# Kernel optimization log

Hardware: AMD Instinct MI355X
Metric: run time of the kernel (lower is better)

## Reference

```python
import jax, jax.numpy as jnp
import numpy as np

N_HEADS = 16


def setup_inputs() -> dict:
    key = jax.random.key(0)
    k1, k2, k3, k4, k5 = jax.random.split(key, 5)
    B, S, D = 2, 2048, 1024
    return {
        "query": jax.random.normal(k1, (B, S, D), dtype=jnp.float32),
        "key": jax.random.normal(k2, (B, S, D), dtype=jnp.float32),
        "value": jax.random.normal(k3, (B, S, D), dtype=jnp.float32),
        "fc_w": jax.random.normal(k4, (D, D), dtype=jnp.float32) * (1.0 / np.sqrt(D)),
        "fc_b": jax.random.normal(k5, (D,), dtype=jnp.float32) * 0.01,
    }


def reference(query, key, value, fc_w, fc_b):
    b, s, d = query.shape
    head_dim = d // N_HEADS
    q = query.reshape(b, s, N_HEADS, head_dim)
    k = key.reshape(b, s, N_HEADS, head_dim)
    v = value.reshape(b, s, N_HEADS, head_dim)
    # energy: [b, n, q, k]
    energy = jnp.einsum('bqnd,bknd->bnqk', q, k)
    scale = 1.0 / jnp.sqrt(jnp.asarray(head_dim, dtype=energy.dtype))
    attn = jax.nn.softmax(energy * scale, axis=3)
    out = jnp.einsum('bnqk,bknd->bqnd', attn, v).reshape(b, s, d)
    # fc: y = x @ W^T + b (torch Linear convention)
    return out @ fc_w.T + fc_b
```

## Files before the change

### kernel.cpp

```cpp
#include <hip/hip_runtime.h>
#include <hip/hip_bf16.h>

#define BATCH 2
#define SEQ 2048
#define DMODEL 1024
#define NHEADS 16
#define HDIM 64
#define KVBLK 64
#define NCHUNK (SEQ / KVBLK)
#define NITER (NCHUNK / 2)

#define QSCALE 0.180336880f
#define DEFER_THR 8.0f

typedef __bf16 bf16x8 __attribute__((ext_vector_type(8)));
typedef __bf16 bf16x4 __attribute__((ext_vector_type(4)));
typedef float f32x4 __attribute__((ext_vector_type(4)));
typedef float f32x16 __attribute__((ext_vector_type(16)));
typedef unsigned int uint2v __attribute__((ext_vector_type(2)));

union B8u { unsigned int u[4]; bf16x8 v; };

__device__ __forceinline__ unsigned int cvt_pk_bf16(float lo, float hi) {
  unsigned int d;
  asm("v_cvt_pk_bf16_f32 %0, %1, %2" : "=v"(d) : "v"(lo), "v"(hi));
  return d;
}

__device__ __forceinline__ void permlane32_swap(unsigned &a, unsigned &b) {
  auto r = __builtin_amdgcn_permlane32_swap(a, b, false, false);
  unsigned tmp[2];
  __builtin_memcpy(tmp, &r, 8);
  a = tmp[0]; b = tmp[1];
}

__global__ __launch_bounds__(256)
void conv_all(const float* __restrict__ K, __bf16* __restrict__ Kbf,
              const float* __restrict__ V, __bf16* __restrict__ Vt,
              const float* __restrict__ W, __bf16* __restrict__ Wbf) {
  const int p = blockIdx.x;
  __shared__ __bf16 T[64][72];

  if (p < 2048) {
    const int t = p * 256 + threadIdx.x;
    const int d8 = t & 7, key = (t >> 3) & (SEQ - 1), g = t >> 14;
    const float* src = K + ((size_t)(g >> 4) * SEQ + key) * DMODEL +
                       (g & 15) * HDIM + d8 * 8;
    f32x4 a = *reinterpret_cast<const f32x4*>(src);
    f32x4 c = *reinterpret_cast<const f32x4*>(src + 4);
    bf16x8 o;
#pragma unroll
    for (int j = 0; j < 4; ++j) { o[j] = (__bf16)a[j]; o[4 + j] = (__bf16)c[j]; }
    *reinterpret_cast<bf16x8*>(Kbf + (size_t)t * 8) = o;
  } else if (p < 3072) {
    const int blk = p - 2048;
    const int g = blk >> 5, c0 = (blk & 31) * 64;
    const int b = g >> 4, h = g & 15;
    {
      const int key = threadIdx.x >> 2, dq = threadIdx.x & 3;
      const float* src = V + ((size_t)(b * SEQ) + c0 + key) * DMODEL +
                         h * HDIM + dq * 16;
#pragma unroll
      for (int i = 0; i < 4; ++i) {
        f32x4 v = *reinterpret_cast<const f32x4*>(src + 4 * i);
        bf16x4 o;
#pragma unroll
        for (int j = 0; j < 4; ++j) o[j] = (__bf16)v[j];
        *reinterpret_cast<bf16x4*>(&T[key][dq * 16 + 4 * i]) = o;
      }
    }
    __syncthreads();
    {
      const int d = threadIdx.x >> 2, kq = threadIdx.x & 3;
      bf16x8 r0, r1;
#pragma unroll
      for (int i = 0; i < 8; ++i) {
        r0[i] = T[kq * 16 + i][d];
        r1[i] = T[kq * 16 + 8 + i][d];
      }
      __bf16* dst = Vt + ((size_t)g * HDIM + d) * SEQ + c0 + kq * 16;
      *reinterpret_cast<bf16x8*>(dst) = r0;
      *reinterpret_cast<bf16x8*>(dst + 8) = r1;
    }
  } else {
    const int t = (p - 3072) * 256 + threadIdx.x;
    f32x4 a = *reinterpret_cast<const f32x4*>(W + (size_t)t * 8);
    f32x4 c = *reinterpret_cast<const f32x4*>(W + (size_t)t * 8 + 4);
    bf16x8 o;
#pragma unroll
    for (int j = 0; j < 4; ++j) { o[j] = (__bf16)a[j]; o[4 + j] = (__bf16)c[j]; }
    *reinterpret_cast<bf16x8*>(Wbf + (size_t)t * 8) = o;
  }
}

__global__ __launch_bounds__(512, 4)
void attn_kernel(const float* __restrict__ Q, const __bf16* __restrict__ Kbf,
                 const __bf16* __restrict__ Vt, __bf16* __restrict__ O) {
  const int p = blockIdx.x;
  const int xcd = p & 7, slot = p >> 3;
  const int g = xcd + 8 * (slot >> 4);
  const int b = g >> 4, h = g & 15;
  const int q0 = (slot & 15) * 128;

  const int tid = threadIdx.x;
  const int wave = tid >> 6, lane = tid & 63;
  const int qg = wave & 3, ks = wave >> 2;
  const int l31 = lane & 31, hi = lane >> 5;
  const int ob = hi << 4;
  const int swz = (l31 & 7) << 4;

  __shared__ __align__(16) __bf16 KsA[2][2][64 * 64];
  __shared__ __align__(16) __bf16 VtA[2][2][64 * 64];

  const int qrow = q0 + (qg << 5) + l31;
  const float* qp = Q + ((size_t)(b * SEQ + qrow)) * DMODEL + h * HDIM;
  bf16x8 qf[4];
#pragma unroll
  for (int kd = 0; kd < 4; ++kd) {
    f32x4 a = *reinterpret_cast<const f32x4*>(qp + kd * 16 + hi * 8);
    f32x4 c = *reinterpret_cast<const f32x4*>(qp + kd * 16 + hi * 8 + 4);
#pragma unroll
    for (int j = 0; j < 4; ++j) {
      qf[kd][j]     = (__bf16)(a[j] * QSCALE);
      qf[kd][4 + j] = (__bf16)(c[j] * QSCALE);
    }
  }

  f32x16 oacc0, oacc1;
#pragma unroll
  for (int r = 0; r < 16; ++r) { oacc0[r] = 0.f; oacc1[r] = 0.f; }
  float m_run = -1e30f, l_run = 0.f;

  const __bf16* kgb = Kbf + (size_t)g * SEQ * HDIM;
  const __bf16* vgb = Vt + (size_t)g * HDIM * SEQ;

  const int t2 = tid & 255;
  const int sk_key = t2 >> 2, sk_dq = t2 & 3;
  const int sv_dim = t2 >> 2, sv_kq = t2 & 3;
  const int ksw = (sk_key & 7) << 4;
  const int vsw = (sv_dim & 7) << 4;

  bf16x8 kr0, kr1, vr0, vr1;

#define STAGE_LOAD(C0)                                                        \
  do {                                                                        \
    const __bf16* kc = kgb + (size_t)(C0 + sk_key) * HDIM + sk_dq * 16;       \
    kr0 = *reinterpret_cast<const bf16x8*>(kc);                               \
    kr1 = *reinterpret_cast<const bf16x8*>(kc + 8);                           \
    const __bf16* vc = vgb + (size_t)sv_dim * SEQ + (C0) + sv_kq * 16;        \
    vr0 = *reinterpret_cast<const bf16x8*>(vc);                               \
    vr1 = *reinterpret_cast<const bf16x8*>(vc + 8);                           \
  } while (0)

#define STAGE_WRITE(B)                                                        \
  do {                                                                        \
    char* kdst = (char*)(&KsA[ks][B][0]) + sk_key * 128;                      \
    *reinterpret_cast<bf16x8*>(kdst + (((sk_dq << 5)) ^ ksw)) = kr0;          \
    *reinterpret_cast<bf16x8*>(kdst + (((sk_dq << 5) | 16) ^ ksw)) = kr1;     \
    char* vdst = (char*)(&VtA[ks][B][0]) + sv_dim * 128;                      \
    *reinterpret_cast<bf16x8*>(vdst + (((sv_kq << 5)) ^ vsw)) = vr0;          \
    *reinterpret_cast<bf16x8*>(vdst + (((sv_kq << 5) | 16) ^ vsw)) = vr1;     \
  } while (0)

  STAGE_LOAD(ks * NITER * KVBLK);
  STAGE_WRITE(0);
  __syncthreads();

  for (int i = 0; i < NITER; ++i) {
    const int cur = i & 1;
    const bool pf = (i + 1 < NITER);
    if (pf) STAGE_LOAD((ks * NITER + i + 1) * KVBLK);

    const char* kb = (const char*)(&KsA[ks][cur][0]);
    const char* vb = (const char*)(&VtA[ks][cur][0]);

    f32x16 s0, s1;
#pragma unroll
    for (int r = 0; r < 16; ++r) { s0[r] = 0.f; s1[r] = 0.f; }
    __builtin_amdgcn_s_setprio(1);
#pragma unroll
    for (int kd = 0; kd < 4; ++kd) {
      bf16x8 a0 = *reinterpret_cast<const bf16x8*>(
          kb + l31 * 128 + (((kd << 5) | ob) ^ swz));
      bf16x8 a1 = *reinterpret_cast<const bf16x8*>(
          kb + (32 + l31) * 128 + (((kd << 5) | ob) ^ swz));
      s0 = __builtin_amdgcn_mfma_f32_32x32x16_bf16(a0, qf[kd], s0, 0, 0, 0);
      s1 = __builtin_amdgcn_mfma_f32_32x32x16_bf16(a1, qf[kd], s1, 0, 0, 0);
    }
    __builtin_amdgcn_s_setprio(0);

    float m8[8];
#pragma unroll
    for (int r = 0; r < 8; ++r)
      m8[r] = fmaxf(fmaxf(s0[r], s0[r + 8]), fmaxf(s1[r], s1[r + 8]));
    float pm = fmaxf(fmaxf(fmaxf(m8[0], m8[1]), fmaxf(m8[2], m8[3])),
                     fmaxf(fmaxf(m8[4], m8[5]), fmaxf(m8[6], m8[7])));
    pm = fmaxf(pm, __shfl_xor(pm, 32, 64));

    if (!__all(pm <= m_run + DEFER_THR)) {
      float mu = fmaxf(m_run, pm);
      float al = __builtin_amdgcn_exp2f(m_run - mu);
      m_run = mu;
      l_run *= al;
#pragma unroll
      for (int r = 0; r < 16; ++r) { oacc0[r] *= al; oacc1[r] *= al; }
    }

#pragma unroll
    for (int r = 0; r < 16; ++r) {
      s0[r] = __builtin_amdgcn_exp2f(s0[r] - m_run);
      s1[r] = __builtin_amdgcn_exp2f(s1[r] - m_run);
    }
    float t8[8];
#pragma unroll
    for (int r = 0; r < 8; ++r)
      t8[r] = (s0[r] + s0[r + 8]) + (s1[r] + s1[r + 8]);
    float ts = ((t8[0] + t8[1]) + (t8[2] + t8[3])) +
               ((t8[4] + t8[5]) + (t8[6] + t8[7]));
    ts += __shfl_xor(ts, 32, 64);
    l_run += ts;

    B8u pfr[4];
#pragma unroll
    for (int kq = 0; kq < 4; ++kq) {
      f32x16 ps = (kq < 2) ? s0 : s1;
      const int r0 = (kq & 1) * 8;
      unsigned lo0 = cvt_pk_bf16(ps[r0 + 0], ps[r0 + 1]);
      unsigned lo1 = cvt_pk_bf16(ps[r0 + 2], ps[r0 + 3]);
      unsigned h0  = cvt_pk_bf16(ps[r0 + 4], ps[r0 + 5]);
      unsigned h1  = cvt_pk_bf16(ps[r0 + 6], ps[r0 + 7]);
      permlane32_swap(lo0, h0);
      permlane32_swap(lo1, h1);
      pfr[kq].u[0] = lo0; pfr[kq].u[1] = lo1;
      pfr[kq].u[2] = h0;  pfr[kq].u[3] = h1;
    }

    __builtin_amdgcn_s_setprio(1);
#pragma unroll
    for (int kq = 0; kq < 4; ++kq) {
      bf16x8 v0 = *reinterpret_cast<const bf16x8*>(
          vb + l31 * 128 + (((kq << 5) | ob) ^ swz));
      bf16x8 v1 = *reinterpret_cast<const bf16x8*>(
          vb + (32 + l31) * 128 + (((kq << 5) | ob) ^ swz));
      oacc0 = __builtin_amdgcn_mfma_f32_32x32x16_bf16(v0, pfr[kq].v, oacc0, 0, 0, 0);
      oacc1 = __builtin_amdgcn_mfma_f32_32x32x16_bf16(v1, pfr[kq].v, oacc1, 0, 0, 0);
    }
    __builtin_amdgcn_s_setprio(0);

    if (pf) STAGE_WRITE(cur ^ 1);
    __syncthreads();
  }

  float* Ob = (float*)&KsA[0][0][0];
  float* mb = (float*)&VtA[0][0][0];
  float* lb = mb + 4 * 32;

  if (ks == 1) {
    if (hi == 0) { mb[qg * 32 + l31] = m_run; lb[qg * 32 + l31] = l_run; }
#pragma unroll
    for (int dt = 0; dt < 2; ++dt) {
      f32x16 oa = dt ? oacc1 : oacc0;
#pragma unroll
      for (int r = 0; r < 16; ++r) {
        int dim = dt * 32 + (r & 3) + 8 * (r >> 2) + 4 * hi;
        Ob[(qg * 64 + dim) * 32 + l31] = oa[r];
      }
    }
  }
  __syncthreads();

  if (ks == 0) {
    float m1 = mb[qg * 32 + l31], l1 = lb[qg * 32 + l31];
    float m = fmaxf(m_run, m1);
    float a0 = __builtin_amdgcn_exp2f(m_run - m);
    float a1 = __builtin_amdgcn_exp2f(m1 - m);
    const float inv = 1.0f / (a0 * l_run + a1 * l1);
    __bf16* op = O + ((size_t)(b * SEQ + qrow)) * DMODEL + h * HDIM;
#pragma unroll
    for (int dt = 0; dt < 2; ++dt) {
      f32x16 oa = dt ? oacc1 : oacc0;
#pragma unroll
      for (int a = 0; a < 4; ++a) {
        float e[4];
#pragma unroll
        for (int j = 0; j < 4; ++j) {
          int r = 4 * a + j;
          int dim = dt * 32 + (r & 3) + 8 * (r >> 2) + 4 * hi;
          float opart = Ob[(qg * 64 + dim) * 32 + l31];
          e[j] = (oa[r] * a0 + opart * a1) * inv;
        }
        uint2v w;
        w[0] = cvt_pk_bf16(e[0], e[1]);
        w[1] = cvt_pk_bf16(e[2], e[3]);
        *reinterpret_cast<uint2v*>((char*)op + (dt * 32 + a * 8 + hi * 4) * 2) = w;
      }
    }
  }
#undef STAGE_LOAD
#undef STAGE_WRITE
}

__global__ __launch_bounds__(256)
void fc_kernel(const __bf16* __restrict__ X, const __bf16* __restrict__ W,
               const float* __restrict__ bias, float* __restrict__ Y) {
  const int p = blockIdx.x;
  const int xcd = p & 7, slot = p >> 3;
  const int m0 = (xcd + 8 * (slot >> 4)) * 128;
  const int n0 = (slot & 15) * 64;

  const int tid = threadIdx.x;
  const int wave = tid >> 6, lane = tid & 63;
  const int g = lane >> 4, lr = lane & 15;
  const int wm = wave >> 1, wn = wave & 1;

  __shared__ __bf16 As[128][72];
  __shared__ __bf16 Bs[64][72];

  f32x4 acc[4][2];
#pragma unroll
  for (int i = 0; i < 4; ++i)
#pragma unroll
    for (int j = 0; j < 2; ++j) acc[i][j] = (f32x4){0.f, 0.f, 0.f, 0.f};

  float bv[2];
#pragma unroll
  for (int j = 0; j < 2; ++j) bv[j] = bias[n0 + wn * 32 + 16 * j + lr];

  const int a_row = tid >> 1, a_k8 = tid & 1;
  const int b_row = tid >> 2, b_k8 = tid & 3;

  bf16x8 av[4], wv[2];

#define FC_LOAD(KK)                                                          \
  do {                                                                       \
    _Pragma("unroll") for (int e = 0; e < 4; ++e) {                          \
      int idx = tid + 256 * e;                                               \
      int row = idx >> 3, k8 = idx & 7;                                      \
      av[e] = *reinterpret_cast<const bf16x8*>(                              \
          X + (size_t)(m0 + row) * DMODEL + (KK) + k8 * 8);                  \
    }                                                                        \
    _Pragma("unroll") for (int e = 0; e < 2; ++e) {                          \
      int idx = tid + 256 * e;                                               \
      int row = idx >> 3, k8 = idx & 7;                                      \
      wv[e] = *reinterpret_cast<const bf16x8*>(                              \
          W + (size_t)(n0 + row) * DMODEL + (KK) + k8 * 8);                  \
    }                                                                        \
  } while (0)

#define FC_WRITE()                                                           \
  do {                                                                       \
    _Pragma("unroll") for (int e = 0; e < 4; ++e) {                          \
      int idx = tid + 256 * e;                                               \
      int row = idx >> 3, k8 = idx & 7;                                      \
      *reinterpret_cast<bf16x8*>(&As[row][k8 * 8]) = av[e];                  \
    }                                                                        \
    _Pragma("unroll") for (int e = 0; e < 2; ++e) {                          \
      int idx = tid + 256 * e;                                               \
      int row = idx >> 3, k8 = idx & 7;                                      \
      *reinterpret_cast<bf16x8*>(&Bs[row][k8 * 8]) = wv[e];                  \
    }                                                                        \
  } while (0)

  FC_LOAD(0);

  for (int kk = 0; kk < DMODEL; kk += 64) {
    __syncthreads();
    FC_WRITE();
    __syncthreads();
    if (kk + 64 < DMODEL) FC_LOAD(kk + 64);

#pragma unroll
    for (int ks2 = 0; ks2 < 2; ++ks2) {
      bf16x8 af[4], bfr[2];
#pragma unroll
      for (int i = 0; i < 4; ++i)
        af[i] = *reinterpret_cast<const bf16x8*>(
            &As[wm * 64 + 16 * i + lr][ks2 * 32 + g * 8]);
#pragma unroll
      for (int j = 0; j < 2; ++j)
        bfr[j] = *reinterpret_cast<const bf16x8*>(
            &Bs[wn * 32 + 16 * j + lr][ks2 * 32 + g * 8]);
#pragma unroll
      for (int i = 0; i < 4; ++i)
#pragma unroll
        for (int j = 0; j < 2; ++j)
          acc[i][j] = __builtin_amdgcn_mfma_f32_16x16x32_bf16(
              af[i], bfr[j], acc[i][j], 0, 0, 0);
    }
  }

#pragma unroll
  for (int i = 0; i < 4; ++i) {
    int m = m0 + wm * 64 + 16 * i + g * 4;
#pragma unroll
    for (int j = 0; j < 2; ++j) {
      int n = n0 + wn * 32 + 16 * j + lr;
      float* yp = Y + (size_t)m * DMODEL + n;
#pragma unroll
      for (int r = 0; r < 4; ++r) yp[(size_t)r * DMODEL] = acc[i][j][r] + bv[j];
    }
  }
#undef FC_LOAD
#undef FC_WRITE
}

extern "C" void kernel_launch(void* const* d_in, const int* in_sizes, int n_in,
                              void* d_out, int out_size, void* d_ws, size_t ws_size,
                              hipStream_t stream) {
  const float* q    = (const float*)d_in[0];
  const float* k    = (const float*)d_in[1];
  const float* v    = (const float*)d_in[2];
  const float* w    = (const float*)d_in[3];
  const float* bias = (const float*)d_in[4];
  float* out = (float*)d_out;

  char* ws = (char*)d_ws;
  __bf16* O   = (__bf16*)(ws);
  __bf16* Kbf = (__bf16*)(ws + (8u << 20));
  __bf16* Vt  = (__bf16*)(ws + (16u << 20));
  __bf16* Wbf = (__bf16*)(ws + (24u << 20));

  conv_all<<<dim3(3584), 256, 0, stream>>>(k, Kbf, v, Vt, w, Wbf);
  attn_kernel<<<dim3(512), 512, 0, stream>>>(q, Kbf, Vt, O);
  fc_kernel<<<dim3(512), 256, 0, stream>>>(O, Wbf, bias, out);
}
```

Measured before the change: 84.63 us.

## Single-buffer K/V shared memory with register prefetch to halve LDS footprint

Replaces the double-buffered K/V shared tiles with a single buffer per KV split. Global loads are prefetched into registers two chunks ahead and written to LDS between two barriers. The m/l merge scratch moves to a small dedicated array. This halves LDS use, from 64KB to 32KB, which could allow more blocks per CU. The cost is an extra __syncthreads per iteration, and the LDS write is now serialized behind compute.

```diff
diff --git a/kernel.cpp b/kernel.cpp
--- a/kernel.cpp
+++ b/kernel.cpp
@@ -109,8 +109,8 @@
   const int ob = hi << 4;
   const int swz = (l31 & 7) << 4;
 
-  __shared__ __align__(16) __bf16 KsA[2][2][64 * 64];
-  __shared__ __align__(16) __bf16 VtA[2][2][64 * 64];
+  __shared__ __align__(16) __bf16 SM[2][2][64 * 64];
+  __shared__ float mlb[2][4][32];
 
   const int qrow = q0 + (qg << 5) + l31;
   const float* qp = Q + ((size_t)(b * SEQ + qrow)) * DMODEL + h * HDIM;
@@ -152,27 +152,24 @@
     vr1 = *reinterpret_cast<const bf16x8*>(vc + 8);                           \
   } while (0)
 
-#define STAGE_WRITE(B)                                                        \
+#define STAGE_WRITE()                                                         \
   do {                                                                        \
-    char* kdst = (char*)(&KsA[ks][B][0]) + sk_key * 128;                      \
+    char* kdst = (char*)(&SM[ks][0][0]) + sk_key * 128;                       \
     *reinterpret_cast<bf16x8*>(kdst + (((sk_dq << 5)) ^ ksw)) = kr0;          \
     *reinterpret_cast<bf16x8*>(kdst + (((sk_dq << 5) | 16) ^ ksw)) = kr1;     \
-    char* vdst = (char*)(&VtA[ks][B][0]) + sv_dim * 128;                      \
+    char* vdst = (char*)(&SM[ks][1][0]) + sv_dim * 128;                       \
     *reinterpret_cast<bf16x8*>(vdst + (((sv_kq << 5)) ^ vsw)) = vr0;          \
     *reinterpret_cast<bf16x8*>(vdst + (((sv_kq << 5) | 16) ^ vsw)) = vr1;     \
   } while (0)
 
   STAGE_LOAD(ks * NITER * KVBLK);
-  STAGE_WRITE(0);
+  STAGE_WRITE();
   __syncthreads();
+  STAGE_LOAD((ks * NITER + 1) * KVBLK);
 
   for (int i = 0; i < NITER; ++i) {
-    const int cur = i & 1;
-    const bool pf = (i + 1 < NITER);
-    if (pf) STAGE_LOAD((ks * NITER + i + 1) * KVBLK);
-
-    const char* kb = (const char*)(&KsA[ks][cur][0]);
-    const char* vb = (const char*)(&VtA[ks][cur][0]);
+    const char* kb = (const char*)(&SM[ks][0][0]);
+    const char* vb = (const char*)(&SM[ks][1][0]);
 
     f32x16 s0, s1;
 #pragma unroll
@@ -247,16 +244,18 @@
     }
     __builtin_amdgcn_s_setprio(0);
 
-    if (pf) STAGE_WRITE(cur ^ 1);
     __syncthreads();
-  }
-
-  float* Ob = (float*)&KsA[0][0][0];
-  float* mb = (float*)&VtA[0][0][0];
-  float* lb = mb + 4 * 32;
+    if (i + 1 < NITER) {
+      STAGE_WRITE();
+      if (i + 2 < NITER) STAGE_LOAD((ks * NITER + i + 2) * KVBLK);
+    }
+    __syncthreads();
+  }
+
+  float* Ob = (float*)&SM[0][0][0];
 
   if (ks == 1) {
-    if (hi == 0) { mb[qg * 32 + l31] = m_run; lb[qg * 32 + l31] = l_run; }
+    if (hi == 0) { mlb[0][qg][l31] = m_run; mlb[1][qg][l31] = l_run; }
 #pragma unroll
     for (int dt = 0; dt < 2; ++dt) {
       f32x16 oa = dt ? oacc1 : oacc0;
@@ -270,7 +269,7 @@
   __syncthreads();
 
   if (ks == 0) {
-    float m1 = mb[qg * 32 + l31], l1 = lb[qg * 32 + l31];
+    float m1 = mlb[0][qg][l31], l1 = mlb[1][qg][l31];
     float m = fmaxf(m_run, m1);
     float a0 = __builtin_amdgcn_exp2f(m_run - m);
     float a1 = __builtin_amdgcn_exp2f(m1 - m);
@@ -325,9 +324,6 @@
   float bv[2];
 #pragma unroll
   for (int j = 0; j < 2; ++j) bv[j] = bias[n0 + wn * 32 + 16 * j + lr];
-
-  const int a_row = tid >> 1, a_k8 = tid & 1;
-  const int b_row = tid >> 2, b_k8 = tid & 3;
 
   bf16x8 av[4], wv[2];
 
```

New measurement: 83.82 us, median of 2. Within noise of the previous version (-1.0%).
